# Kernel optimization log

Hardware: AMD Instinct MI355X
Metric: run time of the kernel (lower is better)

Reference implementation:

```python
import jax, jax.numpy as jnp
import numpy as np

BETA = 1.0

def setup_inputs() -> dict:
    key = jax.random.key(0)
    kX, ks = jax.random.split(key)
    P, N = 8192, 1024
    X = jax.random.normal(kX, (P, N), dtype=jnp.float32)
    s = jax.random.normal(ks, (P - 1, N), dtype=jnp.float32)
    return {"X": X, "s": s}

def reference(X, s):
    # score = softmax(beta * s @ X[:-1]^T, axis=1)  -> (P-1, P-1)
    score = jax.nn.softmax(BETA * jnp.einsum('qn,pn->qp', s, X[:-1]), axis=1)
    # output = score @ X[1:]  -> (P-1, N)
    return jnp.einsum('qp,pn->qn', score, X[1:])
```

## Files before the change

### kernel.cpp

```cpp
#include <hip/hip_runtime.h>
#include <math.h>


#define NQ 8191
#define NK 8191
#define DD 1024
#define BQ 64
#define BK 256
#define KSPLIT 2
#define KHALF 4096
#define ITERS 16
#define NW 8
#define NT 512
#define QKK 31

typedef _Float16 half8 __attribute__((ext_vector_type(8)));
typedef float float4v __attribute__((ext_vector_type(4)));

__global__ void prep_kf(const float* __restrict__ X, _Float16* __restrict__ Kf) {
    int b = blockIdx.x * 256 + threadIdx.x;
    int l  = b & 63;
    int kk = (b >> 6) & 31;
    int g  = b >> 11;
    int row = g * 16 + (l & 15);
    int col = kk * 32 + ((l >> 4) << 3);
    const float4v* src = (const float4v*)&X[(size_t)row * DD + col];
    float4v v0 = src[0], v1 = src[1];
    half8 h;
    h[0]=(_Float16)v0[0]; h[1]=(_Float16)v0[1]; h[2]=(_Float16)v0[2]; h[3]=(_Float16)v0[3];
    h[4]=(_Float16)v1[0]; h[5]=(_Float16)v1[1]; h[6]=(_Float16)v1[2]; h[7]=(_Float16)v1[3];
    *(half8*)&Kf[(size_t)b * 8] = h;
}

__global__ void prep_vf(const float* __restrict__ X, _Float16* __restrict__ Vf) {
    int b = blockIdx.x * 256 + threadIdx.x;
    int l   = b & 63;
    int kkg = (b >> 6) & 255;
    int h   = b >> 14;
    int d    = h * 16 + (l & 15);
    int key0 = kkg * 32 + ((l >> 4) << 3);
    half8 hv;
    #pragma unroll
    for (int e = 0; e < 8; ++e) {
        int row = key0 + e + 1;
        float v = (row < 8192) ? X[(size_t)row * DD + d] : 0.f;
        hv[e] = (_Float16)v;
    }
    *(half8*)&Vf[(size_t)b * 8] = hv;
}

__launch_bounds__(NT, 2)
__global__ void flash(const float* __restrict__ s,
                      const _Float16* __restrict__ Kf,
                      const _Float16* __restrict__ Vf,
                      _Float16* __restrict__ Op,
                      float2* __restrict__ ml) {
    __shared__ _Float16 Qf[4 * QKK * 64 * 8];
    __shared__ _Float16 Pf[4 * 8 * 64 * 8];
    __shared__ float    Rm[NW * BQ];

    const int t  = threadIdx.x;
    const int w  = t >> 6;
    const int l  = t & 63;
    const int ln = l & 15;
    const int q4 = l >> 4;
    const int qt = blockIdx.x >> 1;
    const int ks = blockIdx.x & 1;
    const int q0 = qt * BQ;

    for (int e = t; e < 4 * QKK * 64; e += NT) {
        int ll  = e & 63;
        int rem = e >> 6;
        int kk  = rem % QKK;
        int qf  = rem / QKK;
        int row = qf * 16 + (ll & 15);
        int col = kk * 32 + ((ll >> 4) << 3);
        half8 hv;
        if (q0 + row < NQ) {
            const float4v* src = (const float4v*)&s[(size_t)(q0 + row) * DD + col];
            float4v v0 = src[0], v1 = src[1];
            hv[0]=(_Float16)v0[0]; hv[1]=(_Float16)v0[1]; hv[2]=(_Float16)v0[2]; hv[3]=(_Float16)v0[3];
            hv[4]=(_Float16)v1[0]; hv[5]=(_Float16)v1[1]; hv[6]=(_Float16)v1[2]; hv[7]=(_Float16)v1[3];
        } else {
            #pragma unroll
            for (int j = 0; j < 8; ++j) hv[j] = (_Float16)0.f;
        }
        *(half8*)&Qf[(size_t)e * 8] = hv;
    }
    half8 qreg[4];
    #pragma unroll
    for (int qf = 0; qf < 4; ++qf) {
        int row = qf * 16 + ln;
        int col = QKK * 32 + (q4 << 3);
        half8 hv;
        if (q0 + row < NQ) {
            const float4v* src = (const float4v*)&s[(size_t)(q0 + row) * DD + col];
            float4v v0 = src[0], v1 = src[1];
            hv[0]=(_Float16)v0[0]; hv[1]=(_Float16)v0[1]; hv[2]=(_Float16)v0[2]; hv[3]=(_Float16)v0[3];
            hv[4]=(_Float16)v1[0]; hv[5]=(_Float16)v1[1]; hv[6]=(_Float16)v1[2]; hv[7]=(_Float16)v1[3];
        } else {
            #pragma unroll
            for (int j = 0; j < 8; ++j) hv[j] = (_Float16)0.f;
        }
        qreg[qf] = hv;
    }
    __syncthreads();

    float4v o[4][8];
    #pragma unroll
    for (int qf = 0; qf < 4; ++qf)
        #pragma unroll
        for (int dt = 0; dt < 8; ++dt)
            o[qf][dt] = (float4v){0.f, 0.f, 0.f, 0.f};

    float m_run[16], l_run[16];
    #pragma unroll
    for (int i = 0; i < 16; ++i) { m_run[i] = -INFINITY; l_run[i] = 0.f; }

    const int pbase = w * 512 + q4 * 32 + ((ln >> 3) << 7) + (ln & 7);

    for (int it = 0; it < ITERS; ++it) {
        const _Float16* kp0 = Kf + (size_t)(ks * 256 + it * 16 + w * 2) * 16384 + (size_t)l * 8;
        float4v sa[4][2];
        #pragma unroll
        for (int qf = 0; qf < 4; ++qf) {
            sa[qf][0] = (float4v){0.f, 0.f, 0.f, 0.f};
            sa[qf][1] = (float4v){0.f, 0.f, 0.f, 0.f};
        }
        #pragma unroll 4
        for (int kk = 0; kk < QKK; ++kk) {
            half8 k0 = *(const half8*)(kp0 + kk * 512);
            half8 k1 = *(const half8*)(kp0 + 16384 + kk * 512);
            #pragma unroll
            for (int qf = 0; qf < 4; ++qf) {
                half8 qa = *(const half8*)&Qf[((qf * QKK + kk) * 64 + l) * 8];
                sa[qf][0] = __builtin_amdgcn_mfma_f32_16x16x32_f16(qa, k0, sa[qf][0], 0, 0, 0);
                sa[qf][1] = __builtin_amdgcn_mfma_f32_16x16x32_f16(qa, k1, sa[qf][1], 0, 0, 0);
            }
        }
        {
            half8 k0 = *(const half8*)(kp0 + 31 * 512);
            half8 k1 = *(const half8*)(kp0 + 16384 + 31 * 512);
            #pragma unroll
            for (int qf = 0; qf < 4; ++qf) {
                sa[qf][0] = __builtin_amdgcn_mfma_f32_16x16x32_f16(qreg[qf], k0, sa[qf][0], 0, 0, 0);
                sa[qf][1] = __builtin_amdgcn_mfma_f32_16x16x32_f16(qreg[qf], k1, sa[qf][1], 0, 0, 0);
            }
        }

        const int kbase = ks * KHALF + it * BK + w * 32;
        const bool bad0 = (kbase + ln) >= NK;
        const bool bad1 = (kbase + 16 + ln) >= NK;

        float pm[16];
        #pragma unroll
        for (int qf = 0; qf < 4; ++qf)
            #pragma unroll
            for (int r = 0; r < 4; ++r) {
                float v0 = bad0 ? -INFINITY : sa[qf][0][r];
                float v1 = bad1 ? -INFINITY : sa[qf][1][r];
                pm[qf * 4 + r] = fmaxf(v0, v1);
            }
        #pragma unroll
        for (int i = 0; i < 16; ++i) {
            float v = pm[i];
            v = fmaxf(v, __shfl_xor(v, 1, 64));
            v = fmaxf(v, __shfl_xor(v, 2, 64));
            v = fmaxf(v, __shfl_xor(v, 4, 64));
            v = fmaxf(v, __shfl_xor(v, 8, 64));
            pm[i] = v;
        }
        if (ln == 0) {
            #pragma unroll
            for (int qf = 0; qf < 4; ++qf)
                #pragma unroll
                for (int r = 0; r < 4; ++r)
                    Rm[w * BQ + qf * 16 + q4 * 4 + r] = pm[qf * 4 + r];
        }
        __syncthreads();

        float al[16];
        #pragma unroll
        for (int qf = 0; qf < 4; ++qf)
            #pragma unroll
            for (int r = 0; r < 4; ++r) {
                int row = qf * 16 + q4 * 4 + r;
                int i = qf * 4 + r;
                float v = m_run[i];
                #pragma unroll
                for (int wv = 0; wv < NW; ++wv) v = fmaxf(v, Rm[wv * BQ + row]);
                al[i] = __expf(m_run[i] - v);
                m_run[i] = v;
            }
        #pragma unroll
        for (int i = 0; i < 16; ++i) l_run[i] *= al[i];
        #pragma unroll
        for (int qf = 0; qf < 4; ++qf)
            #pragma unroll
            for (int r = 0; r < 4; ++r) {
                int i = qf * 4 + r;
                float p0 = bad0 ? 0.f : __expf(sa[qf][0][r] - m_run[i]);
                float p1 = bad1 ? 0.f : __expf(sa[qf][1][r] - m_run[i]);
                l_run[i] += p0 + p1;
                Pf[pbase + qf * 4096 + r * 8]       = (_Float16)p0;
                Pf[pbase + qf * 4096 + r * 8 + 256] = (_Float16)p1;
            }
        #pragma unroll
        for (int qf = 0; qf < 4; ++qf)
            #pragma unroll
            for (int dt = 0; dt < 8; ++dt)
                #pragma unroll
                for (int r = 0; r < 4; ++r)
                    o[qf][dt][r] *= al[qf * 4 + r];
        __syncthreads();

        const _Float16* vp = Vf + (size_t)(w * 8) * 131072
                             + (size_t)(ks * 128 + it * 8) * 512 + (size_t)l * 8;
        #pragma unroll 2
        for (int kk2 = 0; kk2 < 8; ++kk2) {
            half8 pa[4];
            #pragma unroll
            for (int qf = 0; qf < 4; ++qf)
                pa[qf] = *(const half8*)&Pf[((qf * 8 + kk2) * 64 + l) * 8];
            #pragma unroll
            for (int dt = 0; dt < 8; ++dt) {
                half8 vf = *(const half8*)(vp + (size_t)dt * 131072 + kk2 * 512);
                #pragma unroll
                for (int qf = 0; qf < 4; ++qf)
                    o[qf][dt] = __builtin_amdgcn_mfma_f32_16x16x32_f16(pa[qf], vf, o[qf][dt], 0, 0, 0);
            }
        }
        __syncthreads();
    }

    float lt[16];
    #pragma unroll
    for (int i = 0; i < 16; ++i) {
        float v = l_run[i];
        v += __shfl_xor(v, 1, 64);
        v += __shfl_xor(v, 2, 64);
        v += __shfl_xor(v, 4, 64);
        v += __shfl_xor(v, 8, 64);
        lt[i] = v;
    }
    if (ln == 0) {
        #pragma unroll
        for (int qf = 0; qf < 4; ++qf)
            #pragma unroll
            for (int r = 0; r < 4; ++r)
                Rm[w * BQ + qf * 16 + q4 * 4 + r] = lt[qf * 4 + r];
    }
    __syncthreads();

    float lsum[16], inv[16];
    #pragma unroll
    for (int qf = 0; qf < 4; ++qf)
        #pragma unroll
        for (int r = 0; r < 4; ++r) {
            int row = qf * 16 + q4 * 4 + r;
            float sum = 0.f;
            #pragma unroll
            for (int wv = 0; wv < NW; ++wv) sum += Rm[wv * BQ + row];
            lsum[qf * 4 + r] = sum;
            inv[qf * 4 + r] = 1.f / sum;
        }

    if (w == 0 && ln == 0) {
        #pragma unroll
        for (int qf = 0; qf < 4; ++qf)
            #pragma unroll
            for (int r = 0; r < 4; ++r) {
                int row = q0 + qf * 16 + q4 * 4 + r;
                int i = qf * 4 + r;
                if (row < NQ)
                    ml[ks * 8192 + row] = make_float2(m_run[i], lsum[i]);
            }
    }

    #pragma unroll
    for (int qf = 0; qf < 4; ++qf)
        #pragma unroll
        for (int dt = 0; dt < 8; ++dt)
            #pragma unroll
            for (int r = 0; r < 4; ++r) {
                int row = q0 + qf * 16 + q4 * 4 + r;
                int col = w * 128 + dt * 16 + ln;
                if (row < NQ)
                    Op[((size_t)ks * NQ + row) * DD + col] =
                        (_Float16)(o[qf][dt][r] * inv[qf * 4 + r]);
            }
}

__global__ void combine(const _Float16* __restrict__ Op,
                        const float2* __restrict__ ml,
                        float* __restrict__ out) {
    size_t idx = ((size_t)blockIdx.x * 256 + threadIdx.x) * 8;
    if (idx >= (size_t)NQ * DD) return;
    int row = (int)(idx >> 10);
    float2 a = ml[row];
    float2 b = ml[8192 + row];
    float m  = fmaxf(a.x, b.x);
    float w0 = a.y * __expf(a.x - m);
    float w1 = b.y * __expf(b.x - m);
    float inv = 1.f / (w0 + w1);
    w0 *= inv; w1 *= inv;
    half8 h0 = *(const half8*)&Op[idx];
    half8 h1 = *(const half8*)&Op[(size_t)NQ * DD + idx];
    float4v o0, o1;
    #pragma unroll
    for (int e = 0; e < 4; ++e) o0[e] = w0 * (float)h0[e] + w1 * (float)h1[e];
    #pragma unroll
    for (int e = 0; e < 4; ++e) o1[e] = w0 * (float)h0[e + 4] + w1 * (float)h1[e + 4];
    *(float4v*)&out[idx]     = o0;
    *(float4v*)&out[idx + 4] = o1;
}

extern "C" void kernel_launch(void* const* d_in, const int* in_sizes, int n_in,
                              void* d_out, int out_size, void* d_ws, size_t ws_size,
                              hipStream_t stream) {
    const float* X = (const float*)d_in[0];
    const float* s = (const float*)d_in[1];
    float* out = (float*)d_out;

    _Float16* Kf = (_Float16*)d_ws;
    _Float16* Vf = Kf + (size_t)8192 * 1024;
    _Float16* Op = Vf + (size_t)8192 * 1024;
    float2*   ml = (float2*)(Op + (size_t)2 * NQ * DD);

    prep_kf<<<4096, 256, 0, stream>>>(X, Kf);
    prep_vf<<<4096, 256, 0, stream>>>(X, Vf);
    flash<<<KSPLIT * ((NQ + BQ - 1) / BQ), NT, 0, stream>>>(s, Kf, Vf, Op, ml);
    combine<<<4096, 256, 0, stream>>>(Op, ml, out);
}
```

Baseline: 683.8 us.

## Software-pipeline K/V global loads with double-buffered registers and remap blocks to XCDs

Replaces the QK and PV inner loops with explicitly double-buffered register prefetch. The next K or V chunk is loaded while the MFMAs run on the current one, and the first K chunk of the next iteration is prefetched during the PV phase. It also remaps block IDs so that blocks on the same XCD share a key half, which should improve L2 reuse of K/V, and transposes the Rm reduction buffer so it can be read with vector LDS loads. Holding the extra K/V buffers raises register pressure, which under launch_bounds(512,2) may cause spills.

```diff
diff --git a/kernel.cpp b/kernel.cpp
--- a/kernel.cpp
+++ b/kernel.cpp
@@ -49,6 +49,43 @@
     *(half8*)&Vf[(size_t)b * 8] = hv;
 }
 
+#define LOADK(BUF, KKBASE)                                                    \
+    _Pragma("unroll")                                                         \
+    for (int j = 0; j < 4; ++j) {                                             \
+        BUF[j][0] = *(const half8*)(kp0 + (KKBASE + j) * 512);                \
+        BUF[j][1] = *(const half8*)(kp0 + 16384 + (KKBASE + j) * 512);        \
+    }
+
+#define MFMAK(BUF, KKBASE)                                                    \
+    _Pragma("unroll")                                                         \
+    for (int j = 0; j < 4; ++j) {                                             \
+        _Pragma("unroll")                                                     \
+        for (int qf = 0; qf < 4; ++qf) {                                      \
+            half8 qa = ((KKBASE + j) == 31) ? qreg[qf]                        \
+                 : *(const half8*)&Qf[((qf * QKK + (KKBASE + j)) * 64 + l) * 8]; \
+            sa[qf][0] = __builtin_amdgcn_mfma_f32_16x16x32_f16(qa, BUF[j][0], sa[qf][0], 0, 0, 0); \
+            sa[qf][1] = __builtin_amdgcn_mfma_f32_16x16x32_f16(qa, BUF[j][1], sa[qf][1], 0, 0, 0); \
+        }                                                                     \
+    }
+
+#define LOADV(BUF, KK2)                                                       \
+    _Pragma("unroll")                                                         \
+    for (int dt = 0; dt < 8; ++dt)                                            \
+        BUF[dt] = *(const half8*)(vp + (size_t)dt * 131072 + (KK2) * 512);
+
+#define MFMAV(BUF, KK2)                                                       \
+    {                                                                         \
+        half8 pa[4];                                                          \
+        _Pragma("unroll")                                                     \
+        for (int qf = 0; qf < 4; ++qf)                                        \
+            pa[qf] = *(const half8*)&Pf[((qf * 8 + (KK2)) * 64 + l) * 8];     \
+        _Pragma("unroll")                                                     \
+        for (int dt = 0; dt < 8; ++dt)                                        \
+            _Pragma("unroll")                                                 \
+            for (int qf = 0; qf < 4; ++qf)                                    \
+                o[qf][dt] = __builtin_amdgcn_mfma_f32_16x16x32_f16(pa[qf], BUF[dt], o[qf][dt], 0, 0, 0); \
+    }
+
 __launch_bounds__(NT, 2)
 __global__ void flash(const float* __restrict__ s,
                       const _Float16* __restrict__ Kf,
@@ -57,16 +94,20 @@
                       float2* __restrict__ ml) {
     __shared__ _Float16 Qf[4 * QKK * 64 * 8];
     __shared__ _Float16 Pf[4 * 8 * 64 * 8];
-    __shared__ float    Rm[NW * BQ];
+    __shared__ float    Rm[BQ * NW];
 
     const int t  = threadIdx.x;
     const int w  = t >> 6;
     const int l  = t & 63;
     const int ln = l & 15;
     const int q4 = l >> 4;
-    const int qt = blockIdx.x >> 1;
-    const int ks = blockIdx.x & 1;
-    const int q0 = qt * BQ;
+
+    const int bid  = blockIdx.x;
+    const int xcd  = bid & 7;
+    const int slot = bid >> 3;
+    const int ks   = xcd & 1;
+    const int qt   = slot * 4 + (xcd >> 1);
+    const int q0   = qt * BQ;
 
     for (int e = t; e < 4 * QKK * 64; e += NT) {
         int ll  = e & 63;
@@ -119,34 +160,33 @@
 
     const int pbase = w * 512 + q4 * 32 + ((ln >> 3) << 7) + (ln & 7);
 
+    half8 kA[4][2], kB[4][2];
+    half8 vA[8], vB[8];
+
+    {
+        const _Float16* kp0 = Kf + (size_t)(ks * 256 + w * 2) * 16384 + (size_t)l * 8;
+        LOADK(kA, 0);
+    }
+
     for (int it = 0; it < ITERS; ++it) {
         const _Float16* kp0 = Kf + (size_t)(ks * 256 + it * 16 + w * 2) * 16384 + (size_t)l * 8;
+        const _Float16* vp  = Vf + (size_t)(w * 8) * 131072
+                              + (size_t)(ks * 128 + it * 8) * 512 + (size_t)l * 8;
+
         float4v sa[4][2];
         #pragma unroll
         for (int qf = 0; qf < 4; ++qf) {
             sa[qf][0] = (float4v){0.f, 0.f, 0.f, 0.f};
             sa[qf][1] = (float4v){0.f, 0.f, 0.f, 0.f};
         }
-        #pragma unroll 4
-        for (int kk = 0; kk < QKK; ++kk) {
-            half8 k0 = *(const half8*)(kp0 + kk * 512);
-            half8 k1 = *(const half8*)(kp0 + 16384 + kk * 512);
-            #pragma unroll
-            for (int qf = 0; qf < 4; ++qf) {
-                half8 qa = *(const half8*)&Qf[((qf * QKK + kk) * 64 + l) * 8];
-                sa[qf][0] = __builtin_amdgcn_mfma_f32_16x16x32_f16(qa, k0, sa[qf][0], 0, 0, 0);
-                sa[qf][1] = __builtin_amdgcn_mfma_f32_16x16x32_f16(qa, k1, sa[qf][1], 0, 0, 0);
-            }
-        }
-        {
-            half8 k0 = *(const half8*)(kp0 + 31 * 512);
-            half8 k1 = *(const half8*)(kp0 + 16384 + 31 * 512);
-            #pragma unroll
-            for (int qf = 0; qf < 4; ++qf) {
-                sa[qf][0] = __builtin_amdgcn_mfma_f32_16x16x32_f16(qreg[qf], k0, sa[qf][0], 0, 0, 0);
-                sa[qf][1] = __builtin_amdgcn_mfma_f32_16x16x32_f16(qreg[qf], k1, sa[qf][1], 0, 0, 0);
-            }
-        }
+        LOADK(kB, 4);   MFMAK(kA, 0);
+        LOADK(kA, 8);   MFMAK(kB, 4);
+        LOADK(kB, 12);  MFMAK(kA, 8);
+        LOADK(kA, 16);  MFMAK(kB, 12);
+        LOADK(kB, 20);  MFMAK(kA, 16);
+        LOADK(kA, 24);  MFMAK(kB, 20);
+        LOADK(kB, 28);  MFMAK(kA, 24);
+        LOADV(vA, 0);   MFMAK(kB, 28);
 
         const int kbase = ks * KHALF + it * BK + w * 32;
         const bool bad0 = (kbase + ln) >= NK;
@@ -175,7 +215,7 @@
             for (int qf = 0; qf < 4; ++qf)
                 #pragma unroll
                 for (int r = 0; r < 4; ++r)
-                    Rm[w * BQ + qf * 16 + q4 * 4 + r] = pm[qf * 4 + r];
+                    Rm[(qf * 16 + q4 * 4 + r) * NW + w] = pm[qf * 4 + r];
         }
         __syncthreads();
 
@@ -186,9 +226,11 @@
             for (int r = 0; r < 4; ++r) {
                 int row = qf * 16 + q4 * 4 + r;
                 int i = qf * 4 + r;
-                float v = m_run[i];
-                #pragma unroll
-                for (int wv = 0; wv < NW; ++wv) v = fmaxf(v, Rm[wv * BQ + row]);
+                float4v ra = *(const float4v*)&Rm[row * NW];
+                float4v rb = *(const float4v*)&Rm[row * NW + 4];
+                float v = fmaxf(fmaxf(fmaxf(ra[0], ra[1]), fmaxf(ra[2], ra[3])),
+                                fmaxf(fmaxf(rb[0], rb[1]), fmaxf(rb[2], rb[3])));
+                v = fmaxf(v, m_run[i]);
                 al[i] = __expf(m_run[i] - v);
                 m_run[i] = v;
             }
@@ -214,22 +256,24 @@
                     o[qf][dt][r] *= al[qf * 4 + r];
         __syncthreads();
 
-        const _Float16* vp = Vf + (size_t)(w * 8) * 131072
-                             + (size_t)(ks * 128 + it * 8) * 512 + (size_t)l * 8;
-        #pragma unroll 2
-        for (int kk2 = 0; kk2 < 8; ++kk2) {
-            half8 pa[4];
-            #pragma unroll
-            for (int qf = 0; qf < 4; ++qf)
-                pa[qf] = *(const half8*)&Pf[((qf * 8 + kk2) * 64 + l) * 8];
-            #pragma unroll
-            for (int dt = 0; dt < 8; ++dt) {
-                half8 vf = *(const half8*)(vp + (size_t)dt * 131072 + kk2 * 512);
-                #pragma unroll
-                for (int qf = 0; qf < 4; ++qf)
-                    o[qf][dt] = __builtin_amdgcn_mfma_f32_16x16x32_f16(pa[qf], vf, o[qf][dt], 0, 0, 0);
-            }
-        }
+        LOADV(vB, 1);  MFMAV(vA, 0);
+        LOADV(vA, 2);  MFMAV(vB, 1);
+        LOADV(vB, 3);  MFMAV(vA, 2);
+        LOADV(vA, 4);  MFMAV(vB, 3);
+        LOADV(vB, 5);  MFMAV(vA, 4);
+        LOADV(vA, 6);  MFMAV(vB, 5);
+        LOADV(vB, 7);  MFMAV(vA, 6);
+        {
+            int itn = (it + 1) & (ITERS - 1);
+            const _Float16* kpn = Kf + (size_t)(ks * 256 + itn * 16 + w * 2) * 16384
+                                  + (size_t)l * 8;
+            #pragma unroll
+            for (int j = 0; j < 4; ++j) {
+                kA[j][0] = *(const half8*)(kpn + j * 512);
+                kA[j][1] = *(const half8*)(kpn + 16384 + j * 512);
+            }
+        }
+        MFMAV(vB, 7);
         __syncthreads();
     }
 
@@ -248,7 +292,7 @@
         for (int qf = 0; qf < 4; ++qf)
             #pragma unroll
             for (int r = 0; r < 4; ++r)
-                Rm[w * BQ + qf * 16 + q4 * 4 + r] = lt[qf * 4 + r];
+                Rm[(qf * 16 + q4 * 4 + r) * NW + w] = lt[qf * 4 + r];
     }
     __syncthreads();
 
@@ -258,9 +302,10 @@
         #pragma unroll
         for (int r = 0; r < 4; ++r) {
             int row = qf * 16 + q4 * 4 + r;
-            float sum = 0.f;
-            #pragma unroll
-            for (int wv = 0; wv < NW; ++wv) sum += Rm[wv * BQ + row];
+            float4v ra = *(const float4v*)&Rm[row * NW];
+            float4v rb = *(const float4v*)&Rm[row * NW + 4];
+            float sum = (ra[0] + ra[1] + ra[2] + ra[3])
+                      + (rb[0] + rb[1] + rb[2] + rb[3]);
             lsum[qf * 4 + r] = sum;
             inv[qf * 4 + r] = 1.f / sum;
         }
```

New measurement: 664.7 us. 2.8% less time.

## Software-pipeline K/V loads via async global-to-LDS copies and stream Q from pre-swizzled buffer

Applied to the files above, without the earlier changes.

Adds a prep kernel that converts and swizzles s into an fp16 MFMA-fragment layout. The flash kernel then streams Q fragments from global memory into registers instead of holding the whole Q tile in LDS. K and V tiles are loaded through global_load_lds into triple and double LDS buffers, with explicit vmcnt waits, so memory latency overlaps the MFMA work, and the next iteration's K and Q are prefetched during the PV phase. The softmax rescale is merged into one loop, and the max/sum scratch is transposed so it can be read with vector loads. In exchange it adds an extra prep pass and workspace, and Q is re-read from global/L2 on every iteration. It also relies on hand-tuned waitcnt counts being correct.

```diff
diff --git a/kernel.cpp b/kernel.cpp
--- a/kernel.cpp
+++ b/kernel.cpp
@@ -12,10 +12,10 @@
 #define ITERS 16
 #define NW 8
 #define NT 512
-#define QKK 31
 
 typedef _Float16 half8 __attribute__((ext_vector_type(8)));
 typedef float float4v __attribute__((ext_vector_type(4)));
+
 
 __global__ void prep_kf(const float* __restrict__ X, _Float16* __restrict__ Kf) {
     int b = blockIdx.x * 256 + threadIdx.x;
@@ -49,62 +49,109 @@
     *(half8*)&Vf[(size_t)b * 8] = hv;
 }
 
+__global__ void prep_qf(const float* __restrict__ s, _Float16* __restrict__ Qg) {
+    int b = blockIdx.x * 256 + threadIdx.x;
+    int l  = b & 63;
+    int kk = (b >> 6) & 31;
+    int qf = (b >> 11) & 3;
+    int qt = b >> 13;
+    int row = qt * 64 + qf * 16 + (l & 15);
+    int col = kk * 32 + ((l >> 4) << 3);
+    half8 hv;
+    if (row < NQ) {
+        const float4v* src = (const float4v*)&s[(size_t)row * DD + col];
+        float4v v0 = src[0], v1 = src[1];
+        hv[0]=(_Float16)v0[0]; hv[1]=(_Float16)v0[1]; hv[2]=(_Float16)v0[2]; hv[3]=(_Float16)v0[3];
+        hv[4]=(_Float16)v1[0]; hv[5]=(_Float16)v1[1]; hv[6]=(_Float16)v1[2]; hv[7]=(_Float16)v1[3];
+    } else {
+        #pragma unroll
+        for (int j = 0; j < 8; ++j) hv[j] = (_Float16)0.f;
+    }
+    *(half8*)&Qg[(size_t)b * 8] = hv;
+}
+
+
+__device__ __forceinline__ void gld16(const _Float16* g, _Float16* lp) {
+    __builtin_amdgcn_global_load_lds(
+        (const __attribute__((address_space(1))) unsigned int*)g,
+        (__attribute__((address_space(3))) unsigned int*)lp, 16, 0, 0);
+}
+
+#define SBAR __builtin_amdgcn_sched_barrier(0)
+#define WAITV(N) do { asm volatile("s_waitcnt vmcnt(" #N ")" ::: "memory"); \
+                      __builtin_amdgcn_sched_barrier(0); } while (0)
+
+#define IK(ARR, GB, kkv) do { \
+    gld16(Kf + ((((size_t)(GB)    ) * 32 + (kkv)) << 9) + (l << 3), &ARR[w][0][0]); \
+    gld16(Kf + ((((size_t)(GB) + 1) * 32 + (kkv)) << 9) + (l << 3), &ARR[w][1][0]); \
+} while (0)
+
+#define IQ(QB, kkv) do { \
+    _Pragma("unroll") \
+    for (int qf_ = 0; qf_ < 4; ++qf_) \
+        QB[qf_] = *(const half8*)(Qg + (((size_t)(qtb4 + qf_) * 32 + (kkv)) << 9) + (l << 3)); \
+} while (0)
+
+#define IV(ARR, hp) do { \
+    _Pragma("unroll") \
+    for (int j_ = 0; j_ < 4; ++j_) \
+        gld16(Vf + (((size_t)(w * 8 + ((hp) & 1) * 4 + j_) * 256 + (kvb + ((hp) >> 1))) << 9) + (l << 3), \
+              &ARR[w][j_][0]); \
+} while (0)
+
+#define P1(kkc, ARR, QB, WAITM) do { \
+    WAITM; \
+    half8 k0_ = *(const half8*)&ARR[w][0][l << 3]; \
+    half8 k1_ = *(const half8*)&ARR[w][1][l << 3]; \
+    _Pragma("unroll") \
+    for (int qf_ = 0; qf_ < 4; ++qf_) { \
+        sa[qf_][0] = __builtin_amdgcn_mfma_f32_16x16x32_f16(QB[qf_], k0_, sa[qf_][0], 0, 0, 0); \
+        sa[qf_][1] = __builtin_amdgcn_mfma_f32_16x16x32_f16(QB[qf_], k1_, sa[qf_][1], 0, 0, 0); \
+    } \
+} while (0)
+
+#define P3(hc, ARR, WAITM) do { \
+    WAITM; \
+    if (((hc) & 1) == 0) { \
+        _Pragma("unroll") \
+        for (int qf_ = 0; qf_ < 4; ++qf_) \
+            pa[qf_] = *(const half8*)&Pf[(((qf_ * 8 + ((hc) >> 1)) * 64 + l) << 3)]; \
+    } \
+    _Pragma("unroll") \
+    for (int j_ = 0; j_ < 4; ++j_) { \
+        half8 vf_ = *(const half8*)&ARR[w][j_][l << 3]; \
+        _Pragma("unroll") \
+        for (int qf_ = 0; qf_ < 4; ++qf_) \
+            o[qf_][((hc) & 1) * 4 + j_] = \
+                __builtin_amdgcn_mfma_f32_16x16x32_f16(pa[qf_], vf_, o[qf_][((hc) & 1) * 4 + j_], 0, 0, 0); \
+    } \
+} while (0)
+
 __launch_bounds__(NT, 2)
-__global__ void flash(const float* __restrict__ s,
+__global__ void flash(const _Float16* __restrict__ Qg,
                       const _Float16* __restrict__ Kf,
                       const _Float16* __restrict__ Vf,
                       _Float16* __restrict__ Op,
                       float2* __restrict__ ml) {
-    __shared__ _Float16 Qf[4 * QKK * 64 * 8];
-    __shared__ _Float16 Pf[4 * 8 * 64 * 8];
-    __shared__ float    Rm[NW * BQ];
+    __shared__ _Float16 KSA[NW][2][512];
+    __shared__ _Float16 KSB[NW][2][512];
+    __shared__ _Float16 KSC[NW][2][512];
+    __shared__ _Float16 VSA[NW][4][512];
+    __shared__ _Float16 VSB[NW][4][512];
+    __shared__ _Float16 Pf[16384];
+    __shared__ float    Rm[BQ * NW];
 
     const int t  = threadIdx.x;
     const int w  = t >> 6;
     const int l  = t & 63;
     const int ln = l & 15;
     const int q4 = l >> 4;
-    const int qt = blockIdx.x >> 1;
-    const int ks = blockIdx.x & 1;
-    const int q0 = qt * BQ;
-
-    for (int e = t; e < 4 * QKK * 64; e += NT) {
-        int ll  = e & 63;
-        int rem = e >> 6;
-        int kk  = rem % QKK;
-        int qf  = rem / QKK;
-        int row = qf * 16 + (ll & 15);
-        int col = kk * 32 + ((ll >> 4) << 3);
-        half8 hv;
-        if (q0 + row < NQ) {
-            const float4v* src = (const float4v*)&s[(size_t)(q0 + row) * DD + col];
-            float4v v0 = src[0], v1 = src[1];
-            hv[0]=(_Float16)v0[0]; hv[1]=(_Float16)v0[1]; hv[2]=(_Float16)v0[2]; hv[3]=(_Float16)v0[3];
-            hv[4]=(_Float16)v1[0]; hv[5]=(_Float16)v1[1]; hv[6]=(_Float16)v1[2]; hv[7]=(_Float16)v1[3];
-        } else {
-            #pragma unroll
-            for (int j = 0; j < 8; ++j) hv[j] = (_Float16)0.f;
-        }
-        *(half8*)&Qf[(size_t)e * 8] = hv;
-    }
-    half8 qreg[4];
-    #pragma unroll
-    for (int qf = 0; qf < 4; ++qf) {
-        int row = qf * 16 + ln;
-        int col = QKK * 32 + (q4 << 3);
-        half8 hv;
-        if (q0 + row < NQ) {
-            const float4v* src = (const float4v*)&s[(size_t)(q0 + row) * DD + col];
-            float4v v0 = src[0], v1 = src[1];
-            hv[0]=(_Float16)v0[0]; hv[1]=(_Float16)v0[1]; hv[2]=(_Float16)v0[2]; hv[3]=(_Float16)v0[3];
-            hv[4]=(_Float16)v1[0]; hv[5]=(_Float16)v1[1]; hv[6]=(_Float16)v1[2]; hv[7]=(_Float16)v1[3];
-        } else {
-            #pragma unroll
-            for (int j = 0; j < 8; ++j) hv[j] = (_Float16)0.f;
-        }
-        qreg[qf] = hv;
-    }
-    __syncthreads();
+
+    const int bid = blockIdx.x;
+    const int qt  = bid >> 1;
+    const int ks  = bid & 1;
+    const int q0  = qt * BQ;
+    const int qtb4 = qt * 4;
 
     float4v o[4][8];
     #pragma unroll
@@ -119,137 +166,137 @@
 
     const int pbase = w * 512 + q4 * 32 + ((ln >> 3) << 7) + (ln & 7);
 
+    half8 qa[4], qb[4], pa[4];
+
+    {
+        const int gk0 = ks * 256 + w * 2;
+        IK(KSA, gk0, 0);
+        IK(KSB, gk0, 1);
+        IK(KSC, gk0, 2);
+        IQ(qa, 0);
+        IQ(qb, 1);
+    }
+    __syncthreads();
+
     for (int it = 0; it < ITERS; ++it) {
-        const _Float16* kp0 = Kf + (size_t)(ks * 256 + it * 16 + w * 2) * 16384 + (size_t)l * 8;
+        const int gk0  = ks * 256 + it * 16 + w * 2;
+        const int itn  = (it + 1) & (ITERS - 1);
+        const int gk0n = ks * 256 + itn * 16 + w * 2;
+        const int kvb  = ks * 128 + it * 8;
+
         float4v sa[4][2];
         #pragma unroll
         for (int qf = 0; qf < 4; ++qf) {
             sa[qf][0] = (float4v){0.f, 0.f, 0.f, 0.f};
             sa[qf][1] = (float4v){0.f, 0.f, 0.f, 0.f};
         }
-        #pragma unroll 4
-        for (int kk = 0; kk < QKK; ++kk) {
-            half8 k0 = *(const half8*)(kp0 + kk * 512);
-            half8 k1 = *(const half8*)(kp0 + 16384 + kk * 512);
-            #pragma unroll
-            for (int qf = 0; qf < 4; ++qf) {
-                half8 qa = *(const half8*)&Qf[((qf * QKK + kk) * 64 + l) * 8];
-                sa[qf][0] = __builtin_amdgcn_mfma_f32_16x16x32_f16(qa, k0, sa[qf][0], 0, 0, 0);
-                sa[qf][1] = __builtin_amdgcn_mfma_f32_16x16x32_f16(qa, k1, sa[qf][1], 0, 0, 0);
-            }
-        }
-        {
-            half8 k0 = *(const half8*)(kp0 + 31 * 512);
-            half8 k1 = *(const half8*)(kp0 + 16384 + 31 * 512);
-            #pragma unroll
-            for (int qf = 0; qf < 4; ++qf) {
-                sa[qf][0] = __builtin_amdgcn_mfma_f32_16x16x32_f16(qreg[qf], k0, sa[qf][0], 0, 0, 0);
-                sa[qf][1] = __builtin_amdgcn_mfma_f32_16x16x32_f16(qreg[qf], k1, sa[qf][1], 0, 0, 0);
-            }
-        }
+
+        P1(0,  KSA, qa, SBAR);    IK(KSA, gk0, 3);  IQ(qa, 2);
+        P1(1,  KSB, qb, SBAR);    IK(KSB, gk0, 4);  IQ(qb, 3);
+        P1(2,  KSC, qa, WAITV(6)); IK(KSC, gk0, 5);  IQ(qa, 4);
+        P1(3,  KSA, qb, WAITV(6)); IK(KSA, gk0, 6);  IQ(qb, 5);
+        P1(4,  KSB, qa, WAITV(6)); IK(KSB, gk0, 7);  IQ(qa, 6);
+        P1(5,  KSC, qb, WAITV(6)); IK(KSC, gk0, 8);  IQ(qb, 7);
+        P1(6,  KSA, qa, WAITV(6)); IK(KSA, gk0, 9);  IQ(qa, 8);
+        P1(7,  KSB, qb, WAITV(6)); IK(KSB, gk0, 10); IQ(qb, 9);
+        P1(8,  KSC, qa, WAITV(6)); IK(KSC, gk0, 11); IQ(qa, 10);
+        P1(9,  KSA, qb, WAITV(6)); IK(KSA, gk0, 12); IQ(qb, 11);
+        P1(10, KSB, qa, WAITV(6)); IK(KSB, gk0, 13); IQ(qa, 12);
+        P1(11, KSC, qb, WAITV(6)); IK(KSC, gk0, 14); IQ(qb, 13);
+        P1(12, KSA, qa, WAITV(6)); IK(KSA, gk0, 15); IQ(qa, 14);
+        P1(13, KSB, qb, WAITV(6)); IK(KSB, gk0, 16); IQ(qb, 15);
+        P1(14, KSC, qa, WAITV(6)); IK(KSC, gk0, 17); IQ(qa, 16);
+        P1(15, KSA, qb, WAITV(6)); IK(KSA, gk0, 18); IQ(qb, 17);
+        P1(16, KSB, qa, WAITV(6)); IK(KSB, gk0, 19); IQ(qa, 18);
+        P1(17, KSC, qb, WAITV(6)); IK(KSC, gk0, 20); IQ(qb, 19);
+        P1(18, KSA, qa, WAITV(6)); IK(KSA, gk0, 21); IQ(qa, 20);
+        P1(19, KSB, qb, WAITV(6)); IK(KSB, gk0, 22); IQ(qb, 21);
+        P1(20, KSC, qa, WAITV(6)); IK(KSC, gk0, 23); IQ(qa, 22);
+        P1(21, KSA, qb, WAITV(6)); IK(KSA, gk0, 24); IQ(qb, 23);
+        P1(22, KSB, qa, WAITV(6)); IK(KSB, gk0, 25); IQ(qa, 24);
+        P1(23, KSC, qb, WAITV(6)); IK(KSC, gk0, 26); IQ(qb, 25);
+        P1(24, KSA, qa, WAITV(6)); IK(KSA, gk0, 27); IQ(qa, 26);
+        P1(25, KSB, qb, WAITV(6)); IK(KSB, gk0, 28); IQ(qb, 27);
+        P1(26, KSC, qa, WAITV(6)); IK(KSC, gk0, 29); IQ(qa, 28);
+        P1(27, KSA, qb, WAITV(6)); IK(KSA, gk0, 30); IQ(qb, 29);
+        P1(28, KSB, qa, WAITV(6)); IK(KSB, gk0, 31); IQ(qa, 30);
+        P1(29, KSC, qb, WAITV(6)); IQ(qb, 31);
+        P1(30, KSA, qa, WAITV(4)); IV(VSA, 0);
+        P1(31, KSB, qb, WAITV(4)); IV(VSB, 1);
 
         const int kbase = ks * KHALF + it * BK + w * 32;
         const bool bad0 = (kbase + ln) >= NK;
         const bool bad1 = (kbase + 16 + ln) >= NK;
 
-        float pm[16];
         #pragma unroll
         for (int qf = 0; qf < 4; ++qf)
             #pragma unroll
             for (int r = 0; r < 4; ++r) {
                 float v0 = bad0 ? -INFINITY : sa[qf][0][r];
                 float v1 = bad1 ? -INFINITY : sa[qf][1][r];
-                pm[qf * 4 + r] = fmaxf(v0, v1);
+                float v = fmaxf(v0, v1);
+                v = fmaxf(v, __shfl_xor(v, 1, 64));
+                v = fmaxf(v, __shfl_xor(v, 2, 64));
+                v = fmaxf(v, __shfl_xor(v, 4, 64));
+                v = fmaxf(v, __shfl_xor(v, 8, 64));
+                if (ln == 0) Rm[(qf * 16 + q4 * 4 + r) * NW + w] = v;
             }
-        #pragma unroll
-        for (int i = 0; i < 16; ++i) {
-            float v = pm[i];
-            v = fmaxf(v, __shfl_xor(v, 1, 64));
-            v = fmaxf(v, __shfl_xor(v, 2, 64));
-            v = fmaxf(v, __shfl_xor(v, 4, 64));
-            v = fmaxf(v, __shfl_xor(v, 8, 64));
-            pm[i] = v;
-        }
-        if (ln == 0) {
-            #pragma unroll
-            for (int qf = 0; qf < 4; ++qf)
-                #pragma unroll
-                for (int r = 0; r < 4; ++r)
-                    Rm[w * BQ + qf * 16 + q4 * 4 + r] = pm[qf * 4 + r];
-        }
         __syncthreads();
 
-        float al[16];
         #pragma unroll
         for (int qf = 0; qf < 4; ++qf)
             #pragma unroll
             for (int r = 0; r < 4; ++r) {
-                int row = qf * 16 + q4 * 4 + r;
-                int i = qf * 4 + r;
-                float v = m_run[i];
-                #pragma unroll
-                for (int wv = 0; wv < NW; ++wv) v = fmaxf(v, Rm[wv * BQ + row]);
-                al[i] = __expf(m_run[i] - v);
-                m_run[i] = v;
-            }
-        #pragma unroll
-        for (int i = 0; i < 16; ++i) l_run[i] *= al[i];
-        #pragma unroll
-        for (int qf = 0; qf < 4; ++qf)
-            #pragma unroll
-            for (int r = 0; r < 4; ++r) {
-                int i = qf * 4 + r;
-                float p0 = bad0 ? 0.f : __expf(sa[qf][0][r] - m_run[i]);
-                float p1 = bad1 ? 0.f : __expf(sa[qf][1][r] - m_run[i]);
-                l_run[i] += p0 + p1;
+                const int i = qf * 4 + r;
+                const int row = qf * 16 + q4 * 4 + r;
+                float4v ra = *(const float4v*)&Rm[row * NW];
+                float4v rb = *(const float4v*)&Rm[row * NW + 4];
+                float mn = fmaxf(fmaxf(fmaxf(ra[0], ra[1]), fmaxf(ra[2], ra[3])),
+                                 fmaxf(fmaxf(rb[0], rb[1]), fmaxf(rb[2], rb[3])));
+                mn = fmaxf(mn, m_run[i]);
+                float al = __expf(m_run[i] - mn);
+                m_run[i] = mn;
+                float p0 = bad0 ? 0.f : __expf(sa[qf][0][r] - mn);
+                float p1 = bad1 ? 0.f : __expf(sa[qf][1][r] - mn);
+                l_run[i] = l_run[i] * al + p0 + p1;
                 Pf[pbase + qf * 4096 + r * 8]       = (_Float16)p0;
                 Pf[pbase + qf * 4096 + r * 8 + 256] = (_Float16)p1;
+                #pragma unroll
+                for (int dt = 0; dt < 8; ++dt) o[qf][dt][r] *= al;
             }
-        #pragma unroll
-        for (int qf = 0; qf < 4; ++qf)
-            #pragma unroll
-            for (int dt = 0; dt < 8; ++dt)
-                #pragma unroll
-                for (int r = 0; r < 4; ++r)
-                    o[qf][dt][r] *= al[qf * 4 + r];
         __syncthreads();
 
-        const _Float16* vp = Vf + (size_t)(w * 8) * 131072
-                             + (size_t)(ks * 128 + it * 8) * 512 + (size_t)l * 8;
-        #pragma unroll 2
-        for (int kk2 = 0; kk2 < 8; ++kk2) {
-            half8 pa[4];
-            #pragma unroll
-            for (int qf = 0; qf < 4; ++qf)
-                pa[qf] = *(const half8*)&Pf[((qf * 8 + kk2) * 64 + l) * 8];
-            #pragma unroll
-            for (int dt = 0; dt < 8; ++dt) {
-                half8 vf = *(const half8*)(vp + (size_t)dt * 131072 + kk2 * 512);
-                #pragma unroll
-                for (int qf = 0; qf < 4; ++qf)
-                    o[qf][dt] = __builtin_amdgcn_mfma_f32_16x16x32_f16(pa[qf], vf, o[qf][dt], 0, 0, 0);
-            }
+        P3(0,  VSA, SBAR);      IV(VSA, 2);
+        P3(1,  VSB, SBAR);      IV(VSB, 3);
+        P3(2,  VSA, WAITV(4));  IV(VSA, 4);
+        P3(3,  VSB, WAITV(4));  IV(VSB, 5);
+        P3(4,  VSA, WAITV(4));  IV(VSA, 6);
+        P3(5,  VSB, WAITV(4));  IV(VSB, 7);
+        P3(6,  VSA, WAITV(4));  IV(VSA, 8);
+        P3(7,  VSB, WAITV(4));  IV(VSB, 9);
+        P3(8,  VSA, WAITV(4));  IV(VSA, 10);
+        P3(9,  VSB, WAITV(4));  IV(VSB, 11);
+        P3(10, VSA, WAITV(4));  IV(VSA, 12);
+        P3(11, VSB, WAITV(4));  IV(VSB, 13);
+        P3(12, VSA, WAITV(4));  IV(VSA, 14);
+        P3(13, VSB, WAITV(4));  IV(VSB, 15); IK(KSA, gk0n, 0); IK(KSB, gk0n, 1);
+        P3(14, VSA, WAITV(8));  IK(KSC, gk0n, 2); IQ(qa, 0);
+        P3(15, VSB, WAITV(10)); IQ(qb, 1);
+
+        __syncthreads();
+    }
+
+    #pragma unroll
+    for (int qf = 0; qf < 4; ++qf)
+        #pragma unroll
+        for (int r = 0; r < 4; ++r) {
+            float v = l_run[qf * 4 + r];
+            v += __shfl_xor(v, 1, 64);
+            v += __shfl_xor(v, 2, 64);
+            v += __shfl_xor(v, 4, 64);
+            v += __shfl_xor(v, 8, 64);
+            if (ln == 0) Rm[(qf * 16 + q4 * 4 + r) * NW + w] = v;
         }
-        __syncthreads();
-    }
-
-    float lt[16];
-    #pragma unroll
-    for (int i = 0; i < 16; ++i) {
-        float v = l_run[i];
-        v += __shfl_xor(v, 1, 64);
-        v += __shfl_xor(v, 2, 64);
-        v += __shfl_xor(v, 4, 64);
-        v += __shfl_xor(v, 8, 64);
-        lt[i] = v;
-    }
-    if (ln == 0) {
-        #pragma unroll
-        for (int qf = 0; qf < 4; ++qf)
-            #pragma unroll
-            for (int r = 0; r < 4; ++r)
-                Rm[w * BQ + qf * 16 + q4 * 4 + r] = lt[qf * 4 + r];
-    }
     __syncthreads();
 
     float lsum[16], inv[16];
@@ -258,9 +305,10 @@
         #pragma unroll
         for (int r = 0; r < 4; ++r) {
             int row = qf * 16 + q4 * 4 + r;
-            float sum = 0.f;
-            #pragma unroll
-            for (int wv = 0; wv < NW; ++wv) sum += Rm[wv * BQ + row];
+            float4v ra = *(const float4v*)&Rm[row * NW];
+            float4v rb = *(const float4v*)&Rm[row * NW + 4];
+            float sum = (ra[0] + ra[1] + ra[2] + ra[3])
+                      + (rb[0] + rb[1] + rb[2] + rb[3]);
             lsum[qf * 4 + r] = sum;
             inv[qf * 4 + r] = 1.f / sum;
         }
@@ -271,9 +319,8 @@
             #pragma unroll
             for (int r = 0; r < 4; ++r) {
                 int row = q0 + qf * 16 + q4 * 4 + r;
-                int i = qf * 4 + r;
                 if (row < NQ)
-                    ml[ks * 8192 + row] = make_float2(m_run[i], lsum[i]);
+                    ml[ks * 8192 + row] = make_float2(m_run[qf * 4 + r], lsum[qf * 4 + r]);
             }
     }
 
@@ -324,11 +371,13 @@
 
     _Float16* Kf = (_Float16*)d_ws;
     _Float16* Vf = Kf + (size_t)8192 * 1024;
-    _Float16* Op = Vf + (size_t)8192 * 1024;
+    _Float16* Qg = Vf + (size_t)8192 * 1024;
+    _Float16* Op = Qg + (size_t)8192 * 1024;
     float2*   ml = (float2*)(Op + (size_t)2 * NQ * DD);
 
     prep_kf<<<4096, 256, 0, stream>>>(X, Kf);
     prep_vf<<<4096, 256, 0, stream>>>(X, Vf);
-    flash<<<KSPLIT * ((NQ + BQ - 1) / BQ), NT, 0, stream>>>(s, Kf, Vf, Op, ml);
+    prep_qf<<<4096, 256, 0, stream>>>(s, Qg);
+    flash<<<KSPLIT * ((NQ + BQ - 1) / BQ), NT, 0, stream>>>(Qg, Kf, Vf, Op, ml);
     combine<<<4096, 256, 0, stream>>>(Op, ml, out);
 }
```

New measurement: 1.201 ms. 75.6% more time.

## Double wave count per block and software-pipeline K and V fragment loads

Applied to the files above, without the earlier changes.

Moves the flash kernel from 8 to 16 waves per block (1024 threads). Each wave now owns 16 keys in the QK phase and 64 output columns in the PV phase, which halves per-wave accumulator registers. K fragments are prefetched four steps ahead in a rotating buffer, and V loads are double-buffered so global loads overlap MFMA work. The per-wave max scratch is transposed so rows can be reduced with vector LDS reads, and Q's register-resident tail grows to two k-steps to fit shared memory. Occupancy drops to one block per CU, and the larger block makes each barrier more expensive.

```diff
diff --git a/kernel.cpp b/kernel.cpp
--- a/kernel.cpp
+++ b/kernel.cpp
@@ -10,9 +10,9 @@
 #define KSPLIT 2
 #define KHALF 4096
 #define ITERS 16
-#define NW 8
-#define NT 512
-#define QKK 31
+#define NW 16
+#define NT 1024
+#define QKK 30
 
 typedef _Float16 half8 __attribute__((ext_vector_type(8)));
 typedef float float4v __attribute__((ext_vector_type(4)));
@@ -49,7 +49,25 @@
     *(half8*)&Vf[(size_t)b * 8] = hv;
 }
 
-__launch_bounds__(NT, 2)
+#define LOADV(BUF, KK2)                                                       \
+    _Pragma("unroll")                                                         \
+    for (int dt = 0; dt < 4; ++dt)                                            \
+        BUF[dt] = *(const half8*)(vp + (size_t)dt * 131072 + (KK2) * 512);
+
+#define MFMAV(BUF, KK2)                                                       \
+    {                                                                         \
+        half8 pa[4];                                                          \
+        _Pragma("unroll")                                                     \
+        for (int qf = 0; qf < 4; ++qf)                                        \
+            pa[qf] = *(const half8*)&Pf[((qf * 8 + (KK2)) * 64 + l) * 8];     \
+        _Pragma("unroll")                                                     \
+        for (int dt = 0; dt < 4; ++dt)                                        \
+            _Pragma("unroll")                                                 \
+            for (int qf = 0; qf < 4; ++qf)                                    \
+                o[qf][dt] = __builtin_amdgcn_mfma_f32_16x16x32_f16(pa[qf], BUF[dt], o[qf][dt], 0, 0, 0); \
+    }
+
+__launch_bounds__(NT, 1)
 __global__ void flash(const float* __restrict__ s,
                       const _Float16* __restrict__ Kf,
                       const _Float16* __restrict__ Vf,
@@ -57,16 +75,18 @@
                       float2* __restrict__ ml) {
     __shared__ _Float16 Qf[4 * QKK * 64 * 8];
     __shared__ _Float16 Pf[4 * 8 * 64 * 8];
-    __shared__ float    Rm[NW * BQ];
+    __shared__ float    Rm[BQ * NW];
 
     const int t  = threadIdx.x;
     const int w  = t >> 6;
     const int l  = t & 63;
     const int ln = l & 15;
     const int q4 = l >> 4;
-    const int qt = blockIdx.x >> 1;
-    const int ks = blockIdx.x & 1;
-    const int q0 = qt * BQ;
+
+    const int bid = blockIdx.x;
+    const int qt  = bid >> 1;
+    const int ks  = bid & 1;
+    const int q0  = qt * BQ;
 
     for (int e = t; e < 4 * QKK * 64; e += NT) {
         int ll  = e & 63;
@@ -87,80 +107,79 @@
         }
         *(half8*)&Qf[(size_t)e * 8] = hv;
     }
-    half8 qreg[4];
-    #pragma unroll
-    for (int qf = 0; qf < 4; ++qf) {
-        int row = qf * 16 + ln;
-        int col = QKK * 32 + (q4 << 3);
-        half8 hv;
-        if (q0 + row < NQ) {
-            const float4v* src = (const float4v*)&s[(size_t)(q0 + row) * DD + col];
-            float4v v0 = src[0], v1 = src[1];
-            hv[0]=(_Float16)v0[0]; hv[1]=(_Float16)v0[1]; hv[2]=(_Float16)v0[2]; hv[3]=(_Float16)v0[3];
-            hv[4]=(_Float16)v1[0]; hv[5]=(_Float16)v1[1]; hv[6]=(_Float16)v1[2]; hv[7]=(_Float16)v1[3];
-        } else {
-            #pragma unroll
-            for (int j = 0; j < 8; ++j) hv[j] = (_Float16)0.f;
-        }
-        qreg[qf] = hv;
-    }
+    half8 qreg[4][2];
+    #pragma unroll
+    for (int qf = 0; qf < 4; ++qf)
+        #pragma unroll
+        for (int kr = 0; kr < 2; ++kr) {
+            int row = qf * 16 + ln;
+            int col = (QKK + kr) * 32 + (q4 << 3);
+            half8 hv;
+            if (q0 + row < NQ) {
+                const float4v* src = (const float4v*)&s[(size_t)(q0 + row) * DD + col];
+                float4v v0 = src[0], v1 = src[1];
+                hv[0]=(_Float16)v0[0]; hv[1]=(_Float16)v0[1]; hv[2]=(_Float16)v0[2]; hv[3]=(_Float16)v0[3];
+                hv[4]=(_Float16)v1[0]; hv[5]=(_Float16)v1[1]; hv[6]=(_Float16)v1[2]; hv[7]=(_Float16)v1[3];
+            } else {
+                #pragma unroll
+                for (int j = 0; j < 8; ++j) hv[j] = (_Float16)0.f;
+            }
+            qreg[qf][kr] = hv;
+        }
     __syncthreads();
 
-    float4v o[4][8];
+    float4v o[4][4];
     #pragma unroll
     for (int qf = 0; qf < 4; ++qf)
         #pragma unroll
-        for (int dt = 0; dt < 8; ++dt)
+        for (int dt = 0; dt < 4; ++dt)
             o[qf][dt] = (float4v){0.f, 0.f, 0.f, 0.f};
 
     float m_run[16], l_run[16];
     #pragma unroll
     for (int i = 0; i < 16; ++i) { m_run[i] = -INFINITY; l_run[i] = 0.f; }
 
-    const int pbase = w * 512 + q4 * 32 + ((ln >> 3) << 7) + (ln & 7);
+    const int pbase = (w >> 1) * 512 + ((w & 1) * 2 + (ln >> 3)) * 128
+                      + q4 * 32 + (ln & 7);
+
+    half8 va[4], vb[4];
 
     for (int it = 0; it < ITERS; ++it) {
-        const _Float16* kp0 = Kf + (size_t)(ks * 256 + it * 16 + w * 2) * 16384 + (size_t)l * 8;
-        float4v sa[4][2];
-        #pragma unroll
-        for (int qf = 0; qf < 4; ++qf) {
-            sa[qf][0] = (float4v){0.f, 0.f, 0.f, 0.f};
-            sa[qf][1] = (float4v){0.f, 0.f, 0.f, 0.f};
-        }
-        #pragma unroll 4
-        for (int kk = 0; kk < QKK; ++kk) {
-            half8 k0 = *(const half8*)(kp0 + kk * 512);
-            half8 k1 = *(const half8*)(kp0 + 16384 + kk * 512);
+        const _Float16* kp0 = Kf + (size_t)(ks * 256 + it * 16 + w) * 16384
+                              + (size_t)l * 8;
+        float4v sa[4];
+        #pragma unroll
+        for (int qf = 0; qf < 4; ++qf)
+            sa[qf] = (float4v){0.f, 0.f, 0.f, 0.f};
+
+        half8 kbuf[4];
+        #pragma unroll
+        for (int j = 0; j < 4; ++j)
+            kbuf[j] = *(const half8*)(kp0 + j * 512);
+
+        #pragma unroll
+        for (int kk = 0; kk < 32; ++kk) {
+            half8 kf8 = kbuf[kk & 3];
+            if (kk + 4 < 32)
+                kbuf[kk & 3] = *(const half8*)(kp0 + (kk + 4) * 512);
             #pragma unroll
             for (int qf = 0; qf < 4; ++qf) {
-                half8 qa = *(const half8*)&Qf[((qf * QKK + kk) * 64 + l) * 8];
-                sa[qf][0] = __builtin_amdgcn_mfma_f32_16x16x32_f16(qa, k0, sa[qf][0], 0, 0, 0);
-                sa[qf][1] = __builtin_amdgcn_mfma_f32_16x16x32_f16(qa, k1, sa[qf][1], 0, 0, 0);
-            }
-        }
-        {
-            half8 k0 = *(const half8*)(kp0 + 31 * 512);
-            half8 k1 = *(const half8*)(kp0 + 16384 + 31 * 512);
-            #pragma unroll
-            for (int qf = 0; qf < 4; ++qf) {
-                sa[qf][0] = __builtin_amdgcn_mfma_f32_16x16x32_f16(qreg[qf], k0, sa[qf][0], 0, 0, 0);
-                sa[qf][1] = __builtin_amdgcn_mfma_f32_16x16x32_f16(qreg[qf], k1, sa[qf][1], 0, 0, 0);
-            }
-        }
-
-        const int kbase = ks * KHALF + it * BK + w * 32;
+                half8 qa = (kk < QKK)
+                    ? *(const half8*)&Qf[((qf * QKK + kk) * 64 + l) * 8]
+                    : qreg[qf][kk - QKK];
+                sa[qf] = __builtin_amdgcn_mfma_f32_16x16x32_f16(qa, kf8, sa[qf], 0, 0, 0);
+            }
+        }
+
+        const int kbase = ks * KHALF + it * BK + w * 16;
         const bool bad0 = (kbase + ln) >= NK;
-        const bool bad1 = (kbase + 16 + ln) >= NK;
 
         float pm[16];
         #pragma unroll
         for (int qf = 0; qf < 4; ++qf)
             #pragma unroll
-            for (int r = 0; r < 4; ++r) {
-                float v0 = bad0 ? -INFINITY : sa[qf][0][r];
-                float v1 = bad1 ? -INFINITY : sa[qf][1][r];
-                pm[qf * 4 + r] = fmaxf(v0, v1);
-            }
+            for (int r = 0; r < 4; ++r)
+                pm[qf * 4 + r] = bad0 ? -INFINITY : sa[qf][r];
         #pragma unroll
         for (int i = 0; i < 16; ++i) {
             float v = pm[i];
@@ -175,10 +194,12 @@
             for (int qf = 0; qf < 4; ++qf)
                 #pragma unroll
                 for (int r = 0; r < 4; ++r)
-                    Rm[w * BQ + qf * 16 + q4 * 4 + r] = pm[qf * 4 + r];
+                    Rm[(qf * 16 + q4 * 4 + r) * NW + w] = pm[qf * 4 + r];
         }
         __syncthreads();
 
+        const _Float16* vp = Vf + (size_t)(w * 4) * 131072
+                             + (size_t)(ks * 128 + it * 8) * 512 + (size_t)l * 8;
         float al[16];
         #pragma unroll
         for (int qf = 0; qf < 4; ++qf)
@@ -186,9 +207,15 @@
             for (int r = 0; r < 4; ++r) {
                 int row = qf * 16 + q4 * 4 + r;
                 int i = qf * 4 + r;
-                float v = m_run[i];
-                #pragma unroll
-                for (int wv = 0; wv < NW; ++wv) v = fmaxf(v, Rm[wv * BQ + row]);
+                float4v ra = *(const float4v*)&Rm[row * NW];
+                float4v rb = *(const float4v*)&Rm[row * NW + 4];
+                float4v rc = *(const float4v*)&Rm[row * NW + 8];
+                float4v rd = *(const float4v*)&Rm[row * NW + 12];
+                float v = fmaxf(fmaxf(fmaxf(ra[0], ra[1]), fmaxf(ra[2], ra[3])),
+                                fmaxf(fmaxf(rb[0], rb[1]), fmaxf(rb[2], rb[3])));
+                v = fmaxf(v, fmaxf(fmaxf(fmaxf(rc[0], rc[1]), fmaxf(rc[2], rc[3])),
+                                   fmaxf(fmaxf(rd[0], rd[1]), fmaxf(rd[2], rd[3]))));
+                v = fmaxf(v, m_run[i]);
                 al[i] = __expf(m_run[i] - v);
                 m_run[i] = v;
             }
@@ -199,37 +226,28 @@
             #pragma unroll
             for (int r = 0; r < 4; ++r) {
                 int i = qf * 4 + r;
-                float p0 = bad0 ? 0.f : __expf(sa[qf][0][r] - m_run[i]);
-                float p1 = bad1 ? 0.f : __expf(sa[qf][1][r] - m_run[i]);
-                l_run[i] += p0 + p1;
-                Pf[pbase + qf * 4096 + r * 8]       = (_Float16)p0;
-                Pf[pbase + qf * 4096 + r * 8 + 256] = (_Float16)p1;
-            }
-        #pragma unroll
-        for (int qf = 0; qf < 4; ++qf)
-            #pragma unroll
-            for (int dt = 0; dt < 8; ++dt)
+                float p0 = bad0 ? 0.f : __expf(sa[qf][r] - m_run[i]);
+                l_run[i] += p0;
+                Pf[pbase + qf * 4096 + r * 8] = (_Float16)p0;
+            }
+        #pragma unroll
+        for (int qf = 0; qf < 4; ++qf)
+            #pragma unroll
+            for (int dt = 0; dt < 4; ++dt)
                 #pragma unroll
                 for (int r = 0; r < 4; ++r)
                     o[qf][dt][r] *= al[qf * 4 + r];
         __syncthreads();
 
-        const _Float16* vp = Vf + (size_t)(w * 8) * 131072
-                             + (size_t)(ks * 128 + it * 8) * 512 + (size_t)l * 8;
-        #pragma unroll 2
-        for (int kk2 = 0; kk2 < 8; ++kk2) {
-            half8 pa[4];
-            #pragma unroll
-            for (int qf = 0; qf < 4; ++qf)
-                pa[qf] = *(const half8*)&Pf[((qf * 8 + kk2) * 64 + l) * 8];
-            #pragma unroll
-            for (int dt = 0; dt < 8; ++dt) {
-                half8 vf = *(const half8*)(vp + (size_t)dt * 131072 + kk2 * 512);
-                #pragma unroll
-                for (int qf = 0; qf < 4; ++qf)
-                    o[qf][dt] = __builtin_amdgcn_mfma_f32_16x16x32_f16(pa[qf], vf, o[qf][dt], 0, 0, 0);
-            }
-        }
+        LOADV(va, 0);
+        LOADV(vb, 1);  MFMAV(va, 0);
+        LOADV(va, 2);  MFMAV(vb, 1);
+        LOADV(vb, 3);  MFMAV(va, 2);
+        LOADV(va, 4);  MFMAV(vb, 3);
+        LOADV(vb, 5);  MFMAV(va, 4);
+        LOADV(va, 6);  MFMAV(vb, 5);
+        LOADV(vb, 7);  MFMAV(va, 6);
+        MFMAV(vb, 7);
         __syncthreads();
     }
 
@@ -248,7 +266,7 @@
         for (int qf = 0; qf < 4; ++qf)
             #pragma unroll
             for (int r = 0; r < 4; ++r)
-                Rm[w * BQ + qf * 16 + q4 * 4 + r] = lt[qf * 4 + r];
+                Rm[(qf * 16 + q4 * 4 + r) * NW + w] = lt[qf * 4 + r];
     }
     __syncthreads();
 
@@ -260,7 +278,7 @@
             int row = qf * 16 + q4 * 4 + r;
             float sum = 0.f;
             #pragma unroll
-            for (int wv = 0; wv < NW; ++wv) sum += Rm[wv * BQ + row];
+            for (int wv = 0; wv < NW; ++wv) sum += Rm[row * NW + wv];
             lsum[qf * 4 + r] = sum;
             inv[qf * 4 + r] = 1.f / sum;
         }
@@ -280,11 +298,11 @@
     #pragma unroll
     for (int qf = 0; qf < 4; ++qf)
         #pragma unroll
-        for (int dt = 0; dt < 8; ++dt)
+        for (int dt = 0; dt < 4; ++dt)
             #pragma unroll
             for (int r = 0; r < 4; ++r) {
                 int row = q0 + qf * 16 + q4 * 4 + r;
-                int col = w * 128 + dt * 16 + ln;
+                int col = w * 64 + dt * 16 + ln;
                 if (row < NQ)
                     Op[((size_t)ks * NQ + row) * DD + col] =
                         (_Float16)(o[qf][dt][r] * inv[qf * 4 + r]);
```

New measurement: 1.509 ms. 121% more time.
